# Optimization experiments

Measured on AMD Instinct MI355X. Metric: run time of the kernel, lower is better.

Reference implementation:

```python
import jax, jax.numpy as jnp
import numpy as np

N, C_IN, H, W = 32, 128, 56, 56
C_OUT, K = 256, 3
STRIDE = (1, 1)
PAD = (1, 1)


def setup_inputs() -> dict:
    key = jax.random.key(0)
    kx, kw = jax.random.split(key)
    x = jax.random.normal(kx, (N, C_IN, H, W), dtype=jnp.float32)
    k = 1.0 / np.sqrt(C_IN * K * K)
    kernels = jax.random.uniform(kw, (C_OUT, C_IN, K, K), dtype=jnp.float32) * (2 * k) - k
    return {"x": x, "kernels": kernels}


def reference(x, kernels):
    # Equivalent to the im2col + matmul conv in the source (zero padding,
    # stride 1, no bias added in the original forward).
    out = jax.lax.conv_general_dilated(
        x, kernels,
        window_strides=STRIDE,
        padding=[(PAD[0], PAD[0]), (PAD[1], PAD[1])],
        dimension_numbers=("NCHW", "OIHW", "NCHW"),
    )
    return out  # (N, C_OUT, H_out, W_out)
```

## Files before the change

### kernel.cpp

```cpp
#include <hip/hip_runtime.h>


#define CIN   128
#define COUT  256
#define HWID  56
#define IMG   (HWID*HWID)
#define NIMG  32
#define CSTR  40
#define BROW  (58*CSTR)

typedef __attribute__((ext_vector_type(8))) short short8;
typedef __attribute__((ext_vector_type(4))) float float4v;

__device__ __forceinline__ unsigned short f2bf(float f) {
    unsigned int u = __builtin_bit_cast(unsigned int, f);
    u += 0x7FFFu + ((u >> 16) & 1u);
    return (unsigned short)(u >> 16);
}

__global__ void prep_w_kernel(const float* __restrict__ w, unsigned short* __restrict__ W2) {
    int o = blockIdx.x * 256 + threadIdx.x;
    int ci_lo = o & 31;
    int co    = (o >> 5) & 255;
    int s     = o >> 13;
    int ci_hi = s / 9;
    int r9    = s - ci_hi * 9;
    W2[o] = f2bf(w[(co * CIN + ci_hi * 32 + ci_lo) * 9 + r9]);
}

__global__ __launch_bounds__(256) void prep_x_kernel(const float* __restrict__ x,
                                                     unsigned short* __restrict__ X2) {
    __shared__ unsigned short Ls[32 * 66];
    int b  = blockIdx.x;
    int pb = b % 49;
    int t  = b / 49;
    int cb = t & 3;
    int n  = t >> 2;
    int p0 = pb * 64, ci0 = cb * 32;

    const float* src = x + ((long)n * CIN + ci0) * IMG + p0;
    #pragma unroll
    for (int it = 0; it < 2; ++it) {
        int flat = it * 256 + threadIdx.x;
        int ci_l = flat >> 4;
        int c4   = flat & 15;
        float4 v = *(const float4*)(src + ci_l * IMG + c4 * 4);
        unsigned int lo = (unsigned int)f2bf(v.x) | ((unsigned int)f2bf(v.y) << 16);
        unsigned int hi = (unsigned int)f2bf(v.z) | ((unsigned int)f2bf(v.w) << 16);
        *(unsigned int*)(&Ls[ci_l * 66 + c4 * 4])     = lo;
        *(unsigned int*)(&Ls[ci_l * 66 + c4 * 4 + 2]) = hi;
    }
    __syncthreads();
    int p_l = threadIdx.x >> 2;
    int c8  = threadIdx.x & 3;
    unsigned short* dst = X2 + ((long)n * IMG + p0) * CIN + ci0;
    short8 o;
    #pragma unroll
    for (int j = 0; j < 8; ++j)
        o[j] = (short)Ls[(c8 * 8 + j) * 66 + p_l];
    *(short8*)(&dst[(long)p_l * CIN + c8 * 8]) = o;
}

#define ISSUE_TILE(CIHI) do {                                                   \
    _Pragma("unroll")                                                           \
    for (int it = 0; it < 4; ++it) {                                            \
        int idx = it * 256 + tid;                     \
        int ci8 = idx & 3;                                                      \
        int rc  = idx >> 2;                          \
        uint4 v = make_uint4(0u, 0u, 0u, 0u);                                   \
        if (rc < 232) {                                                         \
            int r = rc / 58;                                                    \
            int c = rc - r * 58;                                                \
            int h = h0 - 1 + r;                                                 \
            int w = c - 1;                                                      \
            if ((unsigned)h < 56u && (unsigned)w < 56u)                         \
                v = *(const uint4*)(xnb + ((h * HWID + w) * CIN + (CIHI) * 32 + ci8 * 8)); \
        }                                                                       \
        rx[it] = v;                                                             \
    }                                                                           \
} while (0)

__global__ __launch_bounds__(256, 2)
void conv_mfma_kernel(const unsigned short* __restrict__ X2,
                      const unsigned short* __restrict__ W2,
                      float* __restrict__ out) {
    __shared__ __align__(16) unsigned short Bs[4 * BROW];

    const int tid  = threadIdx.x;
    const int lane = tid & 63;
    const int wv   = tid >> 6;
    const int l15  = lane & 15;
    const int quad = lane >> 4;

    const int pt    = blockIdx.x;
    const int n_img = pt / 28;
    const int h0    = (pt % 28) * 2;

    int boff[7];
    #pragma unroll
    for (int n = 0; n < 7; ++n) {
        int p    = n * 16 + l15;
        int prow = (p >= 56) ? 1 : 0;
        int pcol = p - prow * 56;
        boff[n]  = (prow * 58 + pcol) * CSTR + quad * 8;
    }

    const unsigned short* wbase = W2 + (wv * 64 + l15) * 32 + quad * 8;

    float4v acc[4][7];
    #pragma unroll
    for (int m = 0; m < 4; ++m)
        #pragma unroll
        for (int n = 0; n < 7; ++n)
            acc[m][n] = (float4v){0.f, 0.f, 0.f, 0.f};

    const unsigned short* xnb = X2 + (long)n_img * (IMG * CIN);

    uint4 rx[4];
    ISSUE_TILE(0);

    for (int ci_hi = 0; ci_hi < 4; ++ci_hi) {
        __syncthreads();

        #pragma unroll
        for (int it = 0; it < 4; ++it) {
            int idx = it * 256 + tid;
            int rc  = idx >> 2;
            if (rc < 232) {
                int ci8 = idx & 3;
                *(uint4*)(&Bs[rc * CSTR + ci8 * 8]) = rx[it];
            }
        }
        __syncthreads();

        if (ci_hi < 3) ISSUE_TILE(ci_hi + 1);

        #pragma unroll
        for (int khw = 0; khw < 9; ++khw) {
            const int kh = khw / 3, kw = khw - (khw / 3) * 3;
            const int step = ci_hi * 9 + khw;
            short8 a[4], bfr[7];
            #pragma unroll
            for (int m = 0; m < 4; ++m)
                a[m] = *(const short8*)(wbase + step * 8192 + m * 512);
            #pragma unroll
            for (int n = 0; n < 7; ++n)
                bfr[n] = *(const short8*)(&Bs[boff[n] + (kh * 58 + kw) * CSTR]);
            #pragma unroll
            for (int m = 0; m < 4; ++m)
                #pragma unroll
                for (int n = 0; n < 7; ++n)
                    acc[m][n] = __builtin_amdgcn_mfma_f32_16x16x32_bf16(a[m], bfr[n], acc[m][n], 0, 0, 0);
        }
    }

    float* obase = out + (long)n_img * (COUT * IMG) + h0 * HWID;
    #pragma unroll
    for (int m = 0; m < 4; ++m) {
        #pragma unroll
        for (int r = 0; r < 4; ++r) {
            int co = wv * 64 + m * 16 + quad * 4 + r;
            float* orow = obase + (long)co * IMG;
            #pragma unroll
            for (int n = 0; n < 7; ++n)
                orow[n * 16 + l15] = acc[m][n][r];
        }
    }
}

extern "C" void kernel_launch(void* const* d_in, const int* in_sizes, int n_in,
                              void* d_out, int out_size, void* d_ws, size_t ws_size,
                              hipStream_t stream) {
    const float* x  = (const float*)d_in[0];
    const float* wt = (const float*)d_in[1];
    float* out = (float*)d_out;

    unsigned short* X2 = (unsigned short*)d_ws;
    unsigned short* W2 = X2 + (long)NIMG * CIN * IMG;

    prep_x_kernel<<<NIMG * 4 * 49, 256, 0, stream>>>(x, X2);
    prep_w_kernel<<<(COUT * CIN * 9) / 256, 256, 0, stream>>>(wt, W2);
    conv_mfma_kernel<<<896, 256, 0, stream>>>(X2, W2, out);
}
```

Before: 205.0 us.

## Shrink conv tile to 64 pixels, prefetch weights, merge prep kernels

The conv kernel now tiles 64 output pixels per block instead of two full rows (112), giving 1568 blocks with fewer accumulators and occupancy raised to 3 blocks per CU. Weight fragments for the next step are loaded one step ahead to hide global latency. The two prep kernels are fused into one launch. Smaller tiles improve occupancy and load balance but reduce reuse of the weight fragments per MFMA, and pixel tiles now span row boundaries, so the staged 4-row halo covers fewer useful pixels.

```diff
diff --git a/kernel.cpp b/kernel.cpp
--- a/kernel.cpp
+++ b/kernel.cpp
@@ -8,6 +8,7 @@
 #define NIMG  32
 #define CSTR  40
 #define BROW  (58*CSTR)
+#define NXB   (NIMG*4*49)
 
 typedef __attribute__((ext_vector_type(8))) short short8;
 typedef __attribute__((ext_vector_type(4))) float float4v;
@@ -18,19 +19,23 @@
     return (unsigned short)(u >> 16);
 }
 
-__global__ void prep_w_kernel(const float* __restrict__ w, unsigned short* __restrict__ W2) {
-    int o = blockIdx.x * 256 + threadIdx.x;
-    int ci_lo = o & 31;
-    int co    = (o >> 5) & 255;
-    int s     = o >> 13;
-    int ci_hi = s / 9;
-    int r9    = s - ci_hi * 9;
-    W2[o] = f2bf(w[(co * CIN + ci_hi * 32 + ci_lo) * 9 + r9]);
-}
-
-__global__ __launch_bounds__(256) void prep_x_kernel(const float* __restrict__ x,
-                                                     unsigned short* __restrict__ X2) {
+__global__ __launch_bounds__(256) void prep_kernel(const float* __restrict__ x,
+                                                   const float* __restrict__ w,
+                                                   unsigned short* __restrict__ X2,
+                                                   unsigned short* __restrict__ W2) {
     __shared__ unsigned short Ls[32 * 66];
+
+    if (blockIdx.x >= NXB) {
+        int o = (blockIdx.x - NXB) * 256 + threadIdx.x;
+        int ci_lo = o & 31;
+        int co    = (o >> 5) & 255;
+        int s     = o >> 13;
+        int ci_hi = s / 9;
+        int r9    = s - ci_hi * 9;
+        W2[o] = f2bf(w[(co * CIN + ci_hi * 32 + ci_lo) * 9 + r9]);
+        return;
+    }
+
     int b  = blockIdx.x;
     int pb = b % 49;
     int t  = b / 49;
@@ -71,7 +76,7 @@
         if (rc < 232) {                                                         \
             int r = rc / 58;                                                    \
             int c = rc - r * 58;                                                \
-            int h = h0 - 1 + r;                                                 \
+            int h = r0 - 1 + r;                                                 \
             int w = c - 1;                                                      \
             if ((unsigned)h < 56u && (unsigned)w < 56u)                         \
                 v = *(const uint4*)(xnb + ((h * HWID + w) * CIN + (CIHI) * 32 + ci8 * 8)); \
@@ -80,7 +85,7 @@
     }                                                                           \
 } while (0)
 
-__global__ __launch_bounds__(256, 2)
+__global__ __launch_bounds__(256, 3)
 void conv_mfma_kernel(const unsigned short* __restrict__ X2,
                       const unsigned short* __restrict__ W2,
                       float* __restrict__ out) {
@@ -93,31 +98,39 @@
     const int quad = lane >> 4;
 
     const int pt    = blockIdx.x;
-    const int n_img = pt / 28;
-    const int h0    = (pt % 28) * 2;
-
-    int boff[7];
-    #pragma unroll
-    for (int n = 0; n < 7; ++n) {
-        int p    = n * 16 + l15;
-        int prow = (p >= 56) ? 1 : 0;
-        int pcol = p - prow * 56;
+    const int n_img = pt / 49;
+    const int pb    = pt - n_img * 49;
+    const int p0    = pb * 64;
+    const int r0    = p0 / HWID;
+    const int off56 = p0 - r0 * HWID;
+
+    int boff[4];
+    #pragma unroll
+    for (int n = 0; n < 4; ++n) {
+        int pl   = off56 + n * 16 + l15;
+        int prow = (pl >= 56) ? 1 : 0;
+        int pcol = pl - prow * 56;
         boff[n]  = (prow * 58 + pcol) * CSTR + quad * 8;
     }
 
     const unsigned short* wbase = W2 + (wv * 64 + l15) * 32 + quad * 8;
 
-    float4v acc[4][7];
+    float4v acc[4][4];
     #pragma unroll
     for (int m = 0; m < 4; ++m)
         #pragma unroll
-        for (int n = 0; n < 7; ++n)
+        for (int n = 0; n < 4; ++n)
             acc[m][n] = (float4v){0.f, 0.f, 0.f, 0.f};
 
     const unsigned short* xnb = X2 + (long)n_img * (IMG * CIN);
 
     uint4 rx[4];
     ISSUE_TILE(0);
+
+    short8 a[4], an[4];
+    #pragma unroll
+    for (int m = 0; m < 4; ++m)
+        a[m] = *(const short8*)(wbase + 0 * 8192 + m * 512);
 
     for (int ci_hi = 0; ci_hi < 4; ++ci_hi) {
         __syncthreads();
@@ -139,22 +152,29 @@
         for (int khw = 0; khw < 9; ++khw) {
             const int kh = khw / 3, kw = khw - (khw / 3) * 3;
             const int step = ci_hi * 9 + khw;
-            short8 a[4], bfr[7];
+            if (step < 35) {
+                #pragma unroll
+                for (int m = 0; m < 4; ++m)
+                    an[m] = *(const short8*)(wbase + (step + 1) * 8192 + m * 512);
+            }
+            short8 bfr[4];
             #pragma unroll
-            for (int m = 0; m < 4; ++m)
-                a[m] = *(const short8*)(wbase + step * 8192 + m * 512);
-            #pragma unroll
-            for (int n = 0; n < 7; ++n)
+            for (int n = 0; n < 4; ++n)
                 bfr[n] = *(const short8*)(&Bs[boff[n] + (kh * 58 + kw) * CSTR]);
             #pragma unroll
             for (int m = 0; m < 4; ++m)
                 #pragma unroll
-                for (int n = 0; n < 7; ++n)
+                for (int n = 0; n < 4; ++n)
                     acc[m][n] = __builtin_amdgcn_mfma_f32_16x16x32_bf16(a[m], bfr[n], acc[m][n], 0, 0, 0);
+            if (step < 35) {
+                #pragma unroll
+                for (int m = 0; m < 4; ++m)
+                    a[m] = an[m];
+            }
         }
     }
 
-    float* obase = out + (long)n_img * (COUT * IMG) + h0 * HWID;
+    float* obase = out + (long)n_img * (COUT * IMG) + p0;
     #pragma unroll
     for (int m = 0; m < 4; ++m) {
         #pragma unroll
@@ -162,7 +182,7 @@
             int co = wv * 64 + m * 16 + quad * 4 + r;
             float* orow = obase + (long)co * IMG;
             #pragma unroll
-            for (int n = 0; n < 7; ++n)
+            for (int n = 0; n < 4; ++n)
                 orow[n * 16 + l15] = acc[m][n][r];
         }
     }
@@ -178,7 +198,6 @@
     unsigned short* X2 = (unsigned short*)d_ws;
     unsigned short* W2 = X2 + (long)NIMG * CIN * IMG;
 
-    prep_x_kernel<<<NIMG * 4 * 49, 256, 0, stream>>>(x, X2);
-    prep_w_kernel<<<(COUT * CIN * 9) / 256, 256, 0, stream>>>(wt, W2);
-    conv_mfma_kernel<<<896, 256, 0, stream>>>(X2, W2, out);
-}
+    prep_kernel<<<NXB + (COUT * CIN * 9) / 256, 256, 0, stream>>>(x, wt, X2, W2);
+    conv_mfma_kernel<<<NIMG * 49, 256, 0, stream>>>(X2, W2, out);
+}
```

After: 227.4 us. +10.9%, slower.

## Stage full input-channel tile in LDS once and prefetch weights in registers

Applied to the files above, without the earlier changes.

The conv kernel now loads all 128 input channels of the 4x58 input patch into shared memory up front, in place of four double-buffered 32-channel chunks. This removes the per-chunk barriers and LDS stores from the main loop. Weight fragments are prefetched one step ahead in registers, and the two prep kernels are merged into one launch. In exchange, LDS use grows to about 63KB per block, which may limit occupancy and leaves no overlap between the input load and the MFMA work.

```diff
diff --git a/kernel.cpp b/kernel.cpp
--- a/kernel.cpp
+++ b/kernel.cpp
@@ -6,8 +6,8 @@
 #define HWID  56
 #define IMG   (HWID*HWID)
 #define NIMG  32
-#define CSTR  40
-#define BROW  (58*CSTR)
+#define RSTR  136
+#define NXB   (NIMG*4*49)
 
 typedef __attribute__((ext_vector_type(8))) short short8;
 typedef __attribute__((ext_vector_type(4))) float float4v;
@@ -18,19 +18,23 @@
     return (unsigned short)(u >> 16);
 }
 
-__global__ void prep_w_kernel(const float* __restrict__ w, unsigned short* __restrict__ W2) {
-    int o = blockIdx.x * 256 + threadIdx.x;
-    int ci_lo = o & 31;
-    int co    = (o >> 5) & 255;
-    int s     = o >> 13;
-    int ci_hi = s / 9;
-    int r9    = s - ci_hi * 9;
-    W2[o] = f2bf(w[(co * CIN + ci_hi * 32 + ci_lo) * 9 + r9]);
-}
+__global__ __launch_bounds__(256) void prep_kernel(const float* __restrict__ x,
+                                                   const float* __restrict__ w,
+                                                   unsigned short* __restrict__ X2,
+                                                   unsigned short* __restrict__ W2) {
+    __shared__ unsigned short Ls[32 * 66];
 
-__global__ __launch_bounds__(256) void prep_x_kernel(const float* __restrict__ x,
-                                                     unsigned short* __restrict__ X2) {
-    __shared__ unsigned short Ls[32 * 66];
+    if (blockIdx.x >= NXB) {
+        int o = (blockIdx.x - NXB) * 256 + threadIdx.x;
+        int ci_lo = o & 31;
+        int co    = (o >> 5) & 255;
+        int s     = o >> 13;
+        int ci_hi = s / 9;
+        int r9    = s - ci_hi * 9;
+        W2[o] = f2bf(w[(co * CIN + ci_hi * 32 + ci_lo) * 9 + r9]);
+        return;
+    }
+
     int b  = blockIdx.x;
     int pb = b % 49;
     int t  = b / 49;
@@ -61,12 +65,12 @@
     *(short8*)(&dst[(long)p_l * CIN + c8 * 8]) = o;
 }
 
-#define ISSUE_TILE(CIHI) do {                                                   \
+#define STAGE_BATCH(IT0, CNT) do {                                              \
     _Pragma("unroll")                                                           \
-    for (int it = 0; it < 4; ++it) {                                            \
-        int idx = it * 256 + tid;                     \
-        int ci8 = idx & 3;                                                      \
-        int rc  = idx >> 2;                          \
+    for (int it = 0; it < (CNT); ++it) {                                        \
+        int idx  = ((IT0) + it) * 256 + tid;                                    \
+        int ci16 = idx & 15;                                                    \
+        int rc   = idx >> 4;                                                    \
         uint4 v = make_uint4(0u, 0u, 0u, 0u);                                   \
         if (rc < 232) {                                                         \
             int r = rc / 58;                                                    \
@@ -74,9 +78,17 @@
             int h = h0 - 1 + r;                                                 \
             int w = c - 1;                                                      \
             if ((unsigned)h < 56u && (unsigned)w < 56u)                         \
-                v = *(const uint4*)(xnb + ((h * HWID + w) * CIN + (CIHI) * 32 + ci8 * 8)); \
+                v = *(const uint4*)(xnb + ((h * HWID + w) * CIN + ci16 * 8));   \
         }                                                                       \
-        rx[it] = v;                                                             \
+        stbuf[it] = v;                                                          \
+    }                                                                           \
+    _Pragma("unroll")                                                           \
+    for (int it = 0; it < (CNT); ++it) {                                        \
+        int idx  = ((IT0) + it) * 256 + tid;                                    \
+        int ci16 = idx & 15;                                                    \
+        int rc   = idx >> 4;                                                    \
+        if (rc < 232)                                                           \
+            *(uint4*)(&Xs[rc * RSTR + ci16 * 8]) = stbuf[it];                   \
     }                                                                           \
 } while (0)
 
@@ -84,7 +96,7 @@
 void conv_mfma_kernel(const unsigned short* __restrict__ X2,
                       const unsigned short* __restrict__ W2,
                       float* __restrict__ out) {
-    __shared__ __align__(16) unsigned short Bs[4 * BROW];
+    __shared__ __align__(16) unsigned short Xs[232 * RSTR];
 
     const int tid  = threadIdx.x;
     const int lane = tid & 63;
@@ -102,10 +114,19 @@
         int p    = n * 16 + l15;
         int prow = (p >= 56) ? 1 : 0;
         int pcol = p - prow * 56;
-        boff[n]  = (prow * 58 + pcol) * CSTR + quad * 8;
+        boff[n]  = (prow * 58 + pcol) * RSTR + quad * 8;
     }
 
     const unsigned short* wbase = W2 + (wv * 64 + l15) * 32 + quad * 8;
+
+    const unsigned short* xnb = X2 + (long)n_img * (IMG * CIN);
+
+    {
+        uint4 stbuf[8];
+        STAGE_BATCH(0, 8);
+        STAGE_BATCH(8, 7);
+    }
+    __syncthreads();
 
     float4v acc[4][7];
     #pragma unroll
@@ -114,43 +135,36 @@
         for (int n = 0; n < 7; ++n)
             acc[m][n] = (float4v){0.f, 0.f, 0.f, 0.f};
 
-    const unsigned short* xnb = X2 + (long)n_img * (IMG * CIN);
+    short8 a[4], an[4];
+    #pragma unroll
+    for (int m = 0; m < 4; ++m)
+        a[m] = *(const short8*)(wbase + m * 512);
 
-    uint4 rx[4];
-    ISSUE_TILE(0);
-
+    #pragma unroll
     for (int ci_hi = 0; ci_hi < 4; ++ci_hi) {
-        __syncthreads();
-
-        #pragma unroll
-        for (int it = 0; it < 4; ++it) {
-            int idx = it * 256 + tid;
-            int rc  = idx >> 2;
-            if (rc < 232) {
-                int ci8 = idx & 3;
-                *(uint4*)(&Bs[rc * CSTR + ci8 * 8]) = rx[it];
-            }
-        }
-        __syncthreads();
-
-        if (ci_hi < 3) ISSUE_TILE(ci_hi + 1);
-
         #pragma unroll
         for (int khw = 0; khw < 9; ++khw) {
+            const int step = ci_hi * 9 + khw;
             const int kh = khw / 3, kw = khw - (khw / 3) * 3;
-            const int step = ci_hi * 9 + khw;
-            short8 a[4], bfr[7];
-            #pragma unroll
-            for (int m = 0; m < 4; ++m)
-                a[m] = *(const short8*)(wbase + step * 8192 + m * 512);
+            if (step < 35) {
+                #pragma unroll
+                for (int m = 0; m < 4; ++m)
+                    an[m] = *(const short8*)(wbase + (step + 1) * 8192 + m * 512);
+            }
+            short8 bfr[7];
             #pragma unroll
             for (int n = 0; n < 7; ++n)
-                bfr[n] = *(const short8*)(&Bs[boff[n] + (kh * 58 + kw) * CSTR]);
+                bfr[n] = *(const short8*)(&Xs[boff[n] + (kh * 58 + kw) * RSTR + ci_hi * 32]);
             #pragma unroll
             for (int m = 0; m < 4; ++m)
                 #pragma unroll
                 for (int n = 0; n < 7; ++n)
                     acc[m][n] = __builtin_amdgcn_mfma_f32_16x16x32_bf16(a[m], bfr[n], acc[m][n], 0, 0, 0);
+            if (step < 35) {
+                #pragma unroll
+                for (int m = 0; m < 4; ++m)
+                    a[m] = an[m];
+            }
         }
     }
 
@@ -178,7 +192,6 @@
     unsigned short* X2 = (unsigned short*)d_ws;
     unsigned short* W2 = X2 + (long)NIMG * CIN * IMG;
 
-    prep_x_kernel<<<NIMG * 4 * 49, 256, 0, stream>>>(x, X2);
-    prep_w_kernel<<<(COUT * CIN * 9) / 256, 256, 0, stream>>>(wt, W2);
-    conv_mfma_kernel<<<896, 256, 0, stream>>>(X2, W2, out);
+    prep_kernel<<<NXB + (COUT * CIN * 9) / 256, 256, 0, stream>>>(x, wt, X2, W2);
+    conv_mfma_kernel<<<NIMG * 28, 256, 0, stream>>>(X2, W2, out);
 }
```

Result: faster. 187.5 us (-8.5%).
